# Kernel tuning notes

Hardware: AMD Instinct MI355X
Metric: run time of the kernel (lower is better)

Reference implementation:

```python
import math
import jax, jax.numpy as jnp
import numpy as np

D = 512; H = 8; N = 6; DFF = 2048; VS = 32000; VT = 32000
B = 4; S = 1024; T = 1024
EPS = 1e-5


def _pe(length, d):
    pos = jnp.arange(length, dtype=jnp.float32)[:, None]
    div = jnp.exp(jnp.arange(0, d, 2, dtype=jnp.float32) * (-math.log(10000.0) / d))
    pe = jnp.zeros((length, d), jnp.float32)
    pe = pe.at[:, 0::2].set(jnp.sin(pos * div)).at[:, 1::2].set(jnp.cos(pos * div))
    return pe  # [L, D]


def _ln(x, g, b):
    m = x.mean(-1, keepdims=True)
    v = ((x - m) ** 2).mean(-1, keepdims=True)
    return (x - m) / jnp.sqrt(v + EPS) * g + b


def _mha(xq, xkv, w, b, mask):
    # w: [4, D, D], b: [4, D]; mask broadcastable to [B, H, Sq, Sk]
    nb, sq, d = xq.shape
    dk = d // H
    def proj(x, i):
        return (x @ w[i] + b[i]).reshape(x.shape[0], x.shape[1], H, dk).transpose(0, 2, 1, 3)
    q, k, v = proj(xq, 0), proj(xkv, 1), proj(xkv, 2)
    scores = jnp.einsum('bhqd,bhkd->bhqk', q, k) / math.sqrt(dk)
    scores = jnp.where(mask == 0, -1e9, scores)
    p = jax.nn.softmax(scores, axis=-1)
    o = jnp.einsum('bhqk,bhkd->bhqd', p, v).transpose(0, 2, 1, 3).reshape(nb, sq, d)
    return o @ w[3] + b[3]


def _ffn(x, w1, b1, w2, b2):
    return jax.nn.relu(x @ w1 + b1) @ w2 + b2


def _forward(src_emb, tgt_emb,
             enc_attn_w, enc_attn_b, enc_ffn_w1, enc_ffn_b1, enc_ffn_w2, enc_ffn_b2,
             enc_ln_g, enc_ln_b, enc_fg, enc_fb,
             dec_self_w, dec_self_b, dec_src_w, dec_src_b,
             dec_ffn_w1, dec_ffn_b1, dec_ffn_w2, dec_ffn_b2,
             dec_ln_g, dec_ln_b, dec_fg, dec_fb,
             gen_w, gen_b,
             src, tgt, src_mask, tgt_mask):
    # embed + positional encoding (dropout off: eval mode)
    x = src_emb[src] + _pe(src.shape[1], D)[None]
    for i in range(N):
        a = _mha(x, x, enc_attn_w[i], enc_attn_b[i], src_mask)
        x = _ln(x + a, enc_ln_g[i, 0], enc_ln_b[i, 0])
        f = _ffn(x, enc_ffn_w1[i], enc_ffn_b1[i], enc_ffn_w2[i], enc_ffn_b2[i])
        x = _ln(x + f, enc_ln_g[i, 1], enc_ln_b[i, 1])
    memory = _ln(x, enc_fg, enc_fb)

    y = tgt_emb[tgt] + _pe(tgt.shape[1], D)[None]
    for i in range(N):
        a = _mha(y, y, dec_self_w[i], dec_self_b[i], tgt_mask)
        y = _ln(y + a, dec_ln_g[i, 0], dec_ln_b[i, 0])
        a = _mha(y, memory, dec_src_w[i], dec_src_b[i], src_mask)
        y = _ln(y + a, dec_ln_g[i, 1], dec_ln_b[i, 1])
        f = _ffn(y, dec_ffn_w1[i], dec_ffn_b1[i], dec_ffn_w2[i], dec_ffn_b2[i])
        y = _ln(y + f, dec_ln_g[i, 2], dec_ln_b[i, 2])
    y = _ln(y, dec_fg, dec_fb)
    return y @ gen_w + gen_b  # [B, T, VT]


def setup_inputs():
    key = jax.random.key(0)
    ks = iter(jax.random.split(key, 48))
    def w(*shape):
        return jax.random.normal(next(ks), shape, dtype=jnp.float32) * 0.02
    inp = {}
    inp['src_emb'] = w(VS, D)
    inp['tgt_emb'] = w(VT, D)
    inp['enc_attn_w'] = w(N, 4, D, D)
    inp['enc_attn_b'] = jnp.zeros((N, 4, D), jnp.float32)
    inp['enc_ffn_w1'] = w(N, D, DFF)
    inp['enc_ffn_b1'] = jnp.zeros((N, DFF), jnp.float32)
    inp['enc_ffn_w2'] = w(N, DFF, D)
    inp['enc_ffn_b2'] = jnp.zeros((N, D), jnp.float32)
    inp['enc_ln_g'] = jnp.ones((N, 2, D), jnp.float32)
    inp['enc_ln_b'] = jnp.zeros((N, 2, D), jnp.float32)
    inp['enc_fg'] = jnp.ones((D,), jnp.float32)
    inp['enc_fb'] = jnp.zeros((D,), jnp.float32)
    inp['dec_self_w'] = w(N, 4, D, D)
    inp['dec_self_b'] = jnp.zeros((N, 4, D), jnp.float32)
    inp['dec_src_w'] = w(N, 4, D, D)
    inp['dec_src_b'] = jnp.zeros((N, 4, D), jnp.float32)
    inp['dec_ffn_w1'] = w(N, D, DFF)
    inp['dec_ffn_b1'] = jnp.zeros((N, DFF), jnp.float32)
    inp['dec_ffn_w2'] = w(N, DFF, D)
    inp['dec_ffn_b2'] = jnp.zeros((N, D), jnp.float32)
    inp['dec_ln_g'] = jnp.ones((N, 3, D), jnp.float32)
    inp['dec_ln_b'] = jnp.zeros((N, 3, D), jnp.float32)
    inp['dec_fg'] = jnp.ones((D,), jnp.float32)
    inp['dec_fb'] = jnp.zeros((D,), jnp.float32)
    inp['gen_w'] = w(D, VT)
    inp['gen_b'] = jnp.zeros((VT,), jnp.float32)
    inp['src'] = jax.random.randint(next(ks), (B, S), 0, VS)
    inp['tgt'] = jax.random.randint(next(ks), (B, T), 0, VT)
    inp['src_mask'] = jnp.ones((B, 1, 1, S), jnp.int32)
    inp['tgt_mask'] = jnp.tril(jnp.ones((T, T), jnp.int32))[None, None]  # causal [1,1,T,T]
    return inp


def reference(src_emb, tgt_emb, enc_attn_w, enc_attn_b, enc_ffn_w1, enc_ffn_b1,
              enc_ffn_w2, enc_ffn_b2, enc_ln_g, enc_ln_b, enc_fg, enc_fb,
              dec_self_w, dec_self_b, dec_src_w, dec_src_b,
              dec_ffn_w1, dec_ffn_b1, dec_ffn_w2, dec_ffn_b2,
              dec_ln_g, dec_ln_b, dec_fg, dec_fb, gen_w, gen_b,
              src, tgt, src_mask, tgt_mask):
    return _forward(src_emb, tgt_emb, enc_attn_w, enc_attn_b, enc_ffn_w1, enc_ffn_b1,
                    enc_ffn_w2, enc_ffn_b2, enc_ln_g, enc_ln_b, enc_fg, enc_fb,
                    dec_self_w, dec_self_b, dec_src_w, dec_src_b,
                    dec_ffn_w1, dec_ffn_b1, dec_ffn_w2, dec_ffn_b2,
                    dec_ln_g, dec_ln_b, dec_fg, dec_fb, gen_w, gen_b,
                    src, tgt, src_mask, tgt_mask)
```

## Files before the change

kernel.cpp:

```cpp
#include <hip/hip_runtime.h>


typedef __bf16 bf16x8 __attribute__((ext_vector_type(8)));
typedef __bf16 bf16x4 __attribute__((ext_vector_type(4)));
typedef float  f32x4  __attribute__((ext_vector_type(4)));

__device__ __forceinline__ void gload_lds16(const void* g, void* l) {
  __builtin_amdgcn_global_load_lds((__attribute__((address_space(1))) void*)g,
                                   (__attribute__((address_space(3))) void*)l,
                                   16, 0, 0);
}

__device__ __forceinline__ void hard_barrier() {
  asm volatile("" ::: "memory");
  __builtin_amdgcn_sched_barrier(0);
  __builtin_amdgcn_s_barrier();
  __builtin_amdgcn_sched_barrier(0);
  asm volatile("" ::: "memory");
}

__global__ __launch_bounds__(512, 2)
void gemm256_kernel(const __bf16* __restrict__ A, int lda,
                    const __bf16* __restrict__ BT, int ldb,
                    float* __restrict__ C, int ldc,
                    const float* __restrict__ bias, int K)
{
  __shared__ char ldsraw[131072];
  const int tid  = threadIdx.x;
  const int lane = tid & 63, wid = tid >> 6;
  const int wr = wid >> 2, wc = wid & 3;
  const int bm = blockIdx.x * 256, bn = blockIdx.y * 256;

  auto stage = [&](int slot, int kt) {
    const char* Ag = (const char*)A;
    const char* Bg = (const char*)BT;
    char* base = ldsraw + slot * 65536;
    const long long k0b = (long long)kt * 128;
#pragma unroll
    for (int i = 0; i < 4; i++) {
      int t = tid + i * 512;
      int row = t >> 3, cb = (t & 7) << 4;
      int src = cb ^ ((row & 7) << 4);
      gload_lds16(Ag + ((long long)(bm + row) * lda) * 2 + k0b + src, base + t * 16);
    }
#pragma unroll
    for (int i = 0; i < 4; i++) {
      int t = tid + i * 512;
      int row = t >> 3, cb = (t & 7) << 4;
      int src = cb ^ ((row & 7) << 4);
      gload_lds16(Bg + ((long long)(bn + row) * ldb) * 2 + k0b + src,
                  base + 32768 + t * 16);
    }
  };

  f32x4 acc[8][4] = {};
  const int NT = K / 64;

  stage(0, 0);
  stage(1, 1);

  for (int kt = 0; kt < NT; kt++) {
    if (kt < NT - 1) {
      asm volatile("s_waitcnt vmcnt(8)" ::: "memory");
    } else {
      asm volatile("s_waitcnt vmcnt(0)" ::: "memory");
    }
    hard_barrier();
    const char* sA = ldsraw + (kt & 1) * 65536;
    const char* sB = sA + 32768;
#pragma unroll
    for (int q = 0; q < 4; q++) {
      const int qr = q >> 1, qc = q & 1;
      bf16x8 af[4][2], bf[2][2];
#pragma unroll
      for (int i = 0; i < 4; i++) {
        int row = wr * 128 + (qr * 4 + i) * 16 + (lane & 15);
#pragma unroll
        for (int kk = 0; kk < 2; kk++) {
          int g = kk * 64 + (lane >> 4) * 16;
          af[i][kk] = *(const bf16x8*)(sA + row * 128 + (g ^ ((row & 7) << 4)));
        }
      }
#pragma unroll
      for (int j = 0; j < 2; j++) {
        int row = wc * 64 + (qc * 2 + j) * 16 + (lane & 15);
#pragma unroll
        for (int kk = 0; kk < 2; kk++) {
          int g = kk * 64 + (lane >> 4) * 16;
          bf[j][kk] = *(const bf16x8*)(sB + row * 128 + (g ^ ((row & 7) << 4)));
        }
      }
      __builtin_amdgcn_s_barrier();
      asm volatile("s_waitcnt lgkmcnt(0)" ::: "memory");
      __builtin_amdgcn_sched_barrier(0);
      __builtin_amdgcn_s_setprio(1);
#pragma unroll
      for (int kk = 0; kk < 2; kk++)
#pragma unroll
        for (int i = 0; i < 4; i++)
#pragma unroll
          for (int j = 0; j < 2; j++)
            acc[qr * 4 + i][qc * 2 + j] = __builtin_amdgcn_mfma_f32_16x16x32_bf16(
                af[i][kk], bf[j][kk], acc[qr * 4 + i][qc * 2 + j], 0, 0, 0);
      __builtin_amdgcn_s_setprio(0);
    }
    hard_barrier();
    if (kt + 2 < NT) stage(kt & 1, kt + 2);
  }

  float* ct = (float*)ldsraw;
#pragma unroll
  for (int c = 0; c < 4; c++) {
    __syncthreads();
    if (wr == (c >> 1)) {
      const int ib = (c & 1) * 4;
#pragma unroll
      for (int i = 0; i < 4; i++) {
#pragma unroll
        for (int j = 0; j < 4; j++) {
          int lrow = i * 16 + (lane >> 4) * 4;
          int lcol = wc * 64 + j * 16 + (lane & 15);
          float bv = bias[bn + lcol];
#pragma unroll
          for (int r = 0; r < 4; r++)
            ct[(lrow + r) * 260 + lcol] = acc[ib + i][j][r] + bv;
        }
      }
    }
    __syncthreads();
#pragma unroll
    for (int it = 0; it < 8; it++) {
      int idx = tid + it * 512;
      int row = idx >> 6, c4 = (idx & 63) * 4;
      f32x4 v = *(const f32x4*)(ct + row * 260 + c4);
      *(f32x4*)(C + (long long)(bm + c * 64 + row) * ldc + bn + c4) = v;
    }
  }
}

template<int EPI>
__global__ __launch_bounds__(256)
void gemm2_kernel(const __bf16* __restrict__ A, const __bf16* __restrict__ Akv,
                  int lda,
                  const __bf16* __restrict__ BT, int ldb,
                  void* __restrict__ Cv, int ldc,
                  const float* __restrict__ bias, int K,
                  __bf16* __restrict__ qb, __bf16* __restrict__ kb,
                  __bf16* __restrict__ vt)
{
  constexpr int BM = 128, BN = 128, BK = 64;
  constexpr int WM = 64, WN = 64, FM = 4, FN = 4;
  constexpr int SLOT = 2 * BM * BK;
  __shared__ char ldsraw[65536];
  __bf16* lds = (__bf16*)ldsraw;
  const int tid  = threadIdx.x;
  const int lane = tid & 63, wave = tid >> 6;
  const int wr = wave >> 1, wc = wave & 1;
  const int bm = blockIdx.x * BM, bn = blockIdx.y * BN;
  const __bf16* Ause = (EPI == 2 && blockIdx.y >= 4) ? Akv : A;

  auto stage = [&](int slot, int kt) {
    const char* Ag = (const char*)Ause;
    const char* Bg = (const char*)BT;
    char* base = (char*)(lds + slot * SLOT);
    const long long k0b = (long long)kt * (BK * 2);
#pragma unroll
    for (int i = 0; i < 4; i++) {
      int t = tid + i * 256;
      int row = t >> 3, cb = (t & 7) << 4;
      int src = cb ^ ((row & 7) << 4);
      gload_lds16(Ag + ((long long)(bm + row) * lda) * 2 + k0b + src, base + t * 16);
    }
#pragma unroll
    for (int i = 0; i < 4; i++) {
      int t = tid + i * 256;
      int row = t >> 3, cb = (t & 7) << 4;
      int src = cb ^ ((row & 7) << 4);
      gload_lds16(Bg + ((long long)(bn + row) * ldb) * 2 + k0b + src,
                  base + BM * BK * 2 + t * 16);
    }
  };

  f32x4 acc[FM][FN] = {};
  const int NT = K / BK;

  stage(0, 0);
  stage(1, 1);

  for (int t = 0; t < NT; t++) {
    if (t < NT - 1) {
      asm volatile("s_waitcnt vmcnt(8)" ::: "memory");
    } else {
      asm volatile("s_waitcnt vmcnt(0)" ::: "memory");
    }
    hard_barrier();
    const char* sA = (const char*)(lds + (t & 1) * SLOT);
    const char* sB = sA + BM * BK * 2;
#pragma unroll
    for (int kk = 0; kk < 2; kk++) {
      const int g = kk * 64 + (lane >> 4) * 16;
      bf16x8 af[FM], bfr[FN];
#pragma unroll
      for (int i = 0; i < FM; i++) {
        int row = wr * WM + i * 16 + (lane & 15);
        af[i] = *(const bf16x8*)(sA + row * 128 + (g ^ ((row & 7) << 4)));
      }
#pragma unroll
      for (int j = 0; j < FN; j++) {
        int row = wc * WN + j * 16 + (lane & 15);
        bfr[j] = *(const bf16x8*)(sB + row * 128 + (g ^ ((row & 7) << 4)));
      }
      __builtin_amdgcn_s_setprio(1);
#pragma unroll
      for (int i = 0; i < FM; i++)
#pragma unroll
        for (int j = 0; j < FN; j++)
          acc[i][j] = __builtin_amdgcn_mfma_f32_16x16x32_bf16(af[i], bfr[j], acc[i][j], 0, 0, 0);
      __builtin_amdgcn_s_setprio(0);
    }
    hard_barrier();
    if (t + 2 < NT) stage(t & 1, t + 2);
  }

#pragma unroll
  for (int i = 0; i < FM; i++) {
#pragma unroll
    for (int j = 0; j < FN; j++) {
      int row0 = bm + wr * WM + i * 16 + (lane >> 4) * 4;
      int col  = bn + wc * WN + j * 16 + (lane & 15);
      float bv = bias ? bias[col] : 0.f;
      if constexpr (EPI == 2) {
        int z = col >> 9;
        int cw = col & 511;
        int b = row0 >> 10, s = row0 & 1023;
        int h = cw >> 6, dk = cw & 63;
        long long bh = b * 8 + h;
        if (z == 2) {
          bf16x4 vv;
#pragma unroll
          for (int r = 0; r < 4; r++) vv[r] = (__bf16)(acc[i][j][r] + bv);
          *(bf16x4*)(vt + (bh << 16) + (dk << 10) + s) = vv;
        } else {
          __bf16* dst = (z == 0) ? qb : kb;
          float sc = (z == 0) ? 0.125f : 1.0f;
#pragma unroll
          for (int r = 0; r < 4; r++)
            dst[(bh << 16) + ((long long)(s + r) << 6) + dk] = (__bf16)((acc[i][j][r] + bv) * sc);
        }
      } else if constexpr (EPI == 1) {
        __bf16* C = (__bf16*)Cv;
#pragma unroll
        for (int r = 0; r < 4; r++)
          C[(long long)(row0 + r) * ldc + col] = (__bf16)fmaxf(acc[i][j][r] + bv, 0.f);
      } else {
        float* C = (float*)Cv;
#pragma unroll
        for (int r = 0; r < 4; r++)
          C[(long long)(row0 + r) * ldc + col] = acc[i][j][r] + bv;
      }
    }
  }
}

__global__ __launch_bounds__(256)
void gemm_kernel(const __bf16* __restrict__ A, int lda,
                 const __bf16* __restrict__ BT, int ldb,
                 float* __restrict__ C, int ldc,
                 const float* __restrict__ bias, int K)
{
  constexpr int BM = 128, BN = 64, BK = 64;
  constexpr int WM = 64, WN = 32, FM = 4, FN = 2;
  constexpr int LA = (BM * BK) / 2048;
  constexpr int LB = (BN * BK) / 2048;
  constexpr int SLOT = (BM + BN) * BK;
  __shared__ __bf16 lds[3 * SLOT];
  const int tid  = threadIdx.x;
  const int lane = tid & 63, wave = tid >> 6;
  const int wr = wave >> 1, wc = wave & 1;
  const int bm = blockIdx.x * BM, bn = blockIdx.y * BN;

  auto stage = [&](int slot, int kt) {
    const char* Ag = (const char*)A;
    const char* Bg = (const char*)BT;
    char* base = (char*)(lds + slot * SLOT);
    const long long k0b = (long long)kt * (BK * 2);
#pragma unroll
    for (int i = 0; i < LA; i++) {
      int t = tid + i * 256;
      int row = t >> 3, cb = (t & 7) << 4;
      int src = cb ^ ((row & 7) << 4);
      gload_lds16(Ag + ((long long)(bm + row) * lda) * 2 + k0b + src, base + t * 16);
    }
#pragma unroll
    for (int i = 0; i < LB; i++) {
      int t = tid + i * 256;
      int row = t >> 3, cb = (t & 7) << 4;
      int src = cb ^ ((row & 7) << 4);
      gload_lds16(Bg + ((long long)(bn + row) * ldb) * 2 + k0b + src,
                  base + BM * BK * 2 + t * 16);
    }
  };

  f32x4 acc[FM][FN] = {};
  const int NT = K / BK;

  stage(0, 0);
  stage(1, 1);

  for (int t = 0; t < NT; t++) {
    if (t < NT - 1) {
      asm volatile("s_waitcnt vmcnt(6)" ::: "memory");
    } else {
      asm volatile("s_waitcnt vmcnt(0)" ::: "memory");
    }
    hard_barrier();
    if (t + 2 < NT) stage((t + 2) % 3, t + 2);
    const char* sA = (const char*)(lds + (t % 3) * SLOT);
    const char* sB = sA + BM * BK * 2;
#pragma unroll
    for (int kk = 0; kk < 2; kk++) {
      const int g = kk * 64 + (lane >> 4) * 16;
      bf16x8 af[FM], bfr[FN];
#pragma unroll
      for (int i = 0; i < FM; i++) {
        int row = wr * WM + i * 16 + (lane & 15);
        af[i] = *(const bf16x8*)(sA + row * 128 + (g ^ ((row & 7) << 4)));
      }
#pragma unroll
      for (int j = 0; j < FN; j++) {
        int row = wc * WN + j * 16 + (lane & 15);
        bfr[j] = *(const bf16x8*)(sB + row * 128 + (g ^ ((row & 7) << 4)));
      }
      __builtin_amdgcn_s_setprio(1);
#pragma unroll
      for (int i = 0; i < FM; i++)
#pragma unroll
        for (int j = 0; j < FN; j++)
          acc[i][j] = __builtin_amdgcn_mfma_f32_16x16x32_bf16(af[i], bfr[j], acc[i][j], 0, 0, 0);
      __builtin_amdgcn_s_setprio(0);
    }
  }

#pragma unroll
  for (int i = 0; i < FM; i++) {
#pragma unroll
    for (int j = 0; j < FN; j++) {
      int row0 = bm + wr * WM + i * 16 + (lane >> 4) * 4;
      int col  = bn + wc * WN + j * 16 + (lane & 15);
      float bv = bias ? bias[col] : 0.f;
#pragma unroll
      for (int r = 0; r < 4; r++)
        C[(long long)(row0 + r) * ldc + col] = acc[i][j][r] + bv;
    }
  }
}

template<int CAUSAL>
__global__ __launch_bounds__(256)
void flash_kernel(const __bf16* __restrict__ qb, const __bf16* __restrict__ kb,
                  const __bf16* __restrict__ vt, const int* __restrict__ smask,
                  __bf16* __restrict__ Ob)
{
  __shared__ __bf16 lK[2 * 128 * 64];
  __shared__ __bf16 lV[2 * 64 * 128];
  __shared__ __bf16 lP[4][16 * 128];
  const int bh = blockIdx.y;
  const int b = bh >> 3, h = bh & 7;
  const int q0 = blockIdx.x * 64;
  const int tid = threadIdx.x, lane = tid & 63, w = tid >> 6;
  const char* kh = (const char*)(kb + ((long long)bh << 16));
  const char* vh = (const char*)(vt + ((long long)bh << 16));

  auto stageKV = [&](int buf, int t) {
    int k0 = t * 128;
#pragma unroll
    for (int i = 0; i < 4; i++) {
      int c = tid + i * 256;
      int row = c >> 3, cb = (c & 7) << 4;
      int cl = cb ^ ((row & 7) << 4);
      gload_lds16(kh + (long long)(k0 + row) * 128 + cl, (char*)lK + buf * 16384 + c * 16);
    }
#pragma unroll
    for (int i = 0; i < 4; i++) {
      int c = tid + i * 256;
      int row = c >> 4, cb = (c & 15) << 4;
      int cl = cb ^ ((row & 7) << 4);
      gload_lds16(vh + (long long)row * 2048 + (long long)k0 * 2 + cl, (char*)lV + buf * 16384 + c * 16);
    }
  };

  bf16x8 qa[2];
  {
    const __bf16* qrow = qb + ((long long)bh << 16)
                       + (long long)(q0 + w * 16 + (lane & 15)) * 64 + (lane >> 4) * 8;
    qa[0] = *(const bf16x8*)(qrow);
    qa[1] = *(const bf16x8*)(qrow + 32);
  }
  f32x4 oacc[4] = {};
  float m[4], l[4];
#pragma unroll
  for (int r = 0; r < 4; r++) { m[r] = -3e38f; l[r] = 0.f; }

  const int nt = CAUSAL ? (blockIdx.x / 2 + 1) : 8;
  char* lPw = (char*)lP + w * 4096;

  stageKV(0, 0);
  if (nt > 1) stageKV(1, 1);

  for (int t = 0; t < nt; t++) {
    const int k0 = t * 128;
    if (t < nt - 1) {
      asm volatile("s_waitcnt vmcnt(8)" ::: "memory");
    } else {
      asm volatile("s_waitcnt vmcnt(0)" ::: "memory");
    }
    hard_barrier();
    char* cK = (char*)lK + (t & 1) * 16384;
    char* cV = (char*)lV + (t & 1) * 16384;

    f32x4 sf[8];
#pragma unroll
    for (int f = 0; f < 8; f++) {
      int row = f * 16 + (lane & 15);
      f32x4 s = {};
#pragma unroll
      for (int ks = 0; ks < 2; ks++) {
        int cb = ks * 64 + (lane >> 4) * 16;
        bf16x8 kf = *(const bf16x8*)(cK + row * 128 + (cb ^ ((row & 7) << 4)));
        s = __builtin_amdgcn_mfma_f32_16x16x32_bf16(qa[ks], kf, s, 0, 0, 0);
      }
      sf[f] = s;
    }

    if (!CAUSAL) {
#pragma unroll
      for (int f = 0; f < 8; f++) {
        if (smask[b * 1024 + k0 + f * 16 + (lane & 15)] == 0) {
#pragma unroll
          for (int r = 0; r < 4; r++) sf[f][r] = -1e30f;
        }
      }
    } else if (t == nt - 1) {
#pragma unroll
      for (int f = 0; f < 8; f++) {
        int kc = k0 + f * 16 + (lane & 15);
#pragma unroll
        for (int r = 0; r < 4; r++) {
          int qr = q0 + w * 16 + (lane >> 4) * 4 + r;
          if (kc > qr) sf[f][r] = -1e30f;
        }
      }
    }

    float mt[4];
#pragma unroll
    for (int r = 0; r < 4; r++) {
      float v = sf[0][r];
#pragma unroll
      for (int f = 1; f < 8; f++) v = fmaxf(v, sf[f][r]);
      mt[r] = v;
    }
#pragma unroll
    for (int o = 1; o < 16; o <<= 1)
#pragma unroll
      for (int r = 0; r < 4; r++) mt[r] = fmaxf(mt[r], __shfl_xor(mt[r], o));

    bool need = false;
#pragma unroll
    for (int r = 0; r < 4; r++) need = need || (mt[r] > m[r] + 8.f);
    if (__any(need)) {
      float mn[4], cr[4];
#pragma unroll
      for (int r = 0; r < 4; r++) {
        mn[r] = fmaxf(m[r], mt[r]);
        cr[r] = __expf(m[r] - mn[r]);
        m[r]  = mn[r];
        l[r] *= cr[r];
      }
#pragma unroll
      for (int d = 0; d < 4; d++)
#pragma unroll
        for (int r = 0; r < 4; r++) oacc[d][r] *= cr[r];
    }
    float rs[4] = {0.f, 0.f, 0.f, 0.f};
#pragma unroll
    for (int f = 0; f < 8; f++)
#pragma unroll
      for (int r = 0; r < 4; r++) {
        float p = __expf(sf[f][r] - m[r]);
        sf[f][r] = p;
        rs[r] += p;
      }
#pragma unroll
    for (int o = 1; o < 16; o <<= 1)
#pragma unroll
      for (int r = 0; r < 4; r++) rs[r] += __shfl_xor(rs[r], o);
#pragma unroll
    for (int r = 0; r < 4; r++) l[r] += rs[r];

#pragma unroll
    for (int f = 0; f < 8; f++) {
      int colB = f * 32 + (lane & 15) * 2;
#pragma unroll
      for (int r = 0; r < 4; r++) {
        int row = (lane >> 4) * 4 + r;
        *(__bf16*)(lPw + row * 256 + (colB ^ ((row & 7) << 4))) = (__bf16)sf[f][r];
      }
    }
    asm volatile("s_waitcnt lgkmcnt(0)" ::: "memory");

#pragma unroll
    for (int ks = 0; ks < 4; ks++) {
      int prow = lane & 15;
      int cb = ks * 64 + (lane >> 4) * 16;
      bf16x8 pa = *(const bf16x8*)(lPw + prow * 256 + (cb ^ ((prow & 7) << 4)));
#pragma unroll
      for (int d = 0; d < 4; d++) {
        int vrow = d * 16 + (lane & 15);
        bf16x8 vf = *(const bf16x8*)(cV + vrow * 256 + (cb ^ ((vrow & 7) << 4)));
        oacc[d] = __builtin_amdgcn_mfma_f32_16x16x32_bf16(pa, vf, oacc[d], 0, 0, 0);
      }
    }
    hard_barrier();
    if (t + 2 < nt) stageKV(t & 1, t + 2);
  }

  float inv[4];
#pragma unroll
  for (int r = 0; r < 4; r++) inv[r] = 1.f / l[r];
#pragma unroll
  for (int d = 0; d < 4; d++)
#pragma unroll
    for (int r = 0; r < 4; r++) {
      long long row = b * 1024 + q0 + w * 16 + (lane >> 4) * 4 + r;
      Ob[row * 512 + h * 64 + d * 16 + (lane & 15)] = (__bf16)(oacc[d][r] * inv[r]);
    }
}

__global__ void transpose_w_kernel(const float* __restrict__ W, __bf16* __restrict__ WT,
                                   int K, int N)
{
  __shared__ float t[32][33];
  long long mz = (long long)blockIdx.z * K * N;
  W += mz; WT += mz;
  int n0 = blockIdx.x * 32, k0 = blockIdx.y * 32;
  int tx = threadIdx.x, ty = threadIdx.y;
#pragma unroll
  for (int i = 0; i < 32; i += 8)
    t[ty + i][tx] = W[(long long)(k0 + ty + i) * N + (n0 + tx)];
  __syncthreads();
#pragma unroll
  for (int i = 0; i < 32; i += 8)
    WT[(long long)(n0 + ty + i) * K + (k0 + tx)] = (__bf16)t[tx][ty + i];
}

__global__ void embed_kernel(const float* __restrict__ emb, const int* __restrict__ idx,
                             __bf16* __restrict__ Xb)
{
  int row = blockIdx.x;
  int s   = row & 1023;
  int tok = idx[row];
  int d0  = threadIdx.x * 4;
  float4 e = *(const float4*)(emb + (long long)tok * 512 + d0);
  const float* ep = (const float*)&e;
  bf16x4 ob;
#pragma unroll
  for (int j = 0; j < 4; j++) {
    int d = d0 + j;
    float div = expf((float)(d & ~1) * (-9.210340371976184f / 512.f));
    float ang = (float)s * div;
    float pe  = (d & 1) ? cosf(ang) : sinf(ang);
    ob[j] = (__bf16)(ep[j] + pe);
  }
  *(bf16x4*)(Xb + (long long)row * 512 + d0) = ob;
}

__global__ void ln_kernel(const __bf16* __restrict__ Xin, const float* __restrict__ Rin,
                          const float* __restrict__ g, const float* __restrict__ b,
                          __bf16* __restrict__ Xbout)
{
  int row = blockIdx.x, lane = threadIdx.x;
  long long base = (long long)row * 512 + lane * 8;
  bf16x8 xv = *(const bf16x8*)(Xin + base);
  float x[8];
#pragma unroll
  for (int i = 0; i < 8; i++) x[i] = (float)xv[i];
  if (Rin) {
    float4 r0 = *(const float4*)(Rin + base);
    float4 r1 = *(const float4*)(Rin + base + 4);
    x[0] += r0.x; x[1] += r0.y; x[2] += r0.z; x[3] += r0.w;
    x[4] += r1.x; x[5] += r1.y; x[6] += r1.z; x[7] += r1.w;
  }
  float s = 0.f;
#pragma unroll
  for (int i = 0; i < 8; i++) s += x[i];
#pragma unroll
  for (int o = 32; o > 0; o >>= 1) s += __shfl_xor(s, o);
  float mean = s * (1.f / 512.f);
  float v = 0.f;
#pragma unroll
  for (int i = 0; i < 8; i++) { x[i] -= mean; v += x[i] * x[i]; }
#pragma unroll
  for (int o = 32; o > 0; o >>= 1) v += __shfl_xor(v, o);
  float inv = rsqrtf(v * (1.f / 512.f) + 1e-5f);
  int d0 = lane * 8;
  float gg[8], bb[8];
  *(float4*)gg       = *(const float4*)(g + d0);
  *(float4*)(gg + 4) = *(const float4*)(g + d0 + 4);
  *(float4*)bb       = *(const float4*)(b + d0);
  *(float4*)(bb + 4) = *(const float4*)(b + d0 + 4);
  bf16x8 yb;
#pragma unroll
  for (int i = 0; i < 8; i++)
    yb[i] = (__bf16)(x[i] * inv * gg[i] + bb[i]);
  *(bf16x8*)(Xbout + base) = yb;
}

extern "C" void kernel_launch(void* const* d_in, const int* in_sizes, int n_in,
                              void* d_out, int out_size, void* d_ws, size_t ws_size,
                              hipStream_t stream)
{
  (void)in_sizes; (void)n_in; (void)out_size; (void)ws_size;
  const float* src_emb    = (const float*)d_in[0];
  const float* tgt_emb    = (const float*)d_in[1];
  const float* enc_attn_w = (const float*)d_in[2];
  const float* enc_attn_b = (const float*)d_in[3];
  const float* enc_ffn_w1 = (const float*)d_in[4];
  const float* enc_ffn_b1 = (const float*)d_in[5];
  const float* enc_ffn_w2 = (const float*)d_in[6];
  const float* enc_ffn_b2 = (const float*)d_in[7];
  const float* enc_ln_g   = (const float*)d_in[8];
  const float* enc_ln_b   = (const float*)d_in[9];
  const float* enc_fg     = (const float*)d_in[10];
  const float* enc_fb     = (const float*)d_in[11];
  const float* dec_self_w = (const float*)d_in[12];
  const float* dec_self_b = (const float*)d_in[13];
  const float* dec_src_w  = (const float*)d_in[14];
  const float* dec_src_b  = (const float*)d_in[15];
  const float* dec_ffn_w1 = (const float*)d_in[16];
  const float* dec_ffn_b1 = (const float*)d_in[17];
  const float* dec_ffn_w2 = (const float*)d_in[18];
  const float* dec_ffn_b2 = (const float*)d_in[19];
  const float* dec_ln_g   = (const float*)d_in[20];
  const float* dec_ln_b   = (const float*)d_in[21];
  const float* dec_fg     = (const float*)d_in[22];
  const float* dec_fb     = (const float*)d_in[23];
  const float* gen_w      = (const float*)d_in[24];
  const float* gen_b      = (const float*)d_in[25];
  const int*   src        = (const int*)d_in[26];
  const int*   tgt        = (const int*)d_in[27];
  const int*   src_mask   = (const int*)d_in[28];

  float* out = (float*)d_out;

  char* wp = (char*)d_ws;
  auto alloc = [&](size_t bytes) { void* p = (void*)wp; wp += (bytes + 255) & ~(size_t)255; return p; };
  __bf16* TWea = (__bf16*)alloc(24ull * 262144 * 2);
  __bf16* TWe1 = (__bf16*)alloc(6ull * 1048576 * 2);
  __bf16* TWe2 = (__bf16*)alloc(6ull * 1048576 * 2);
  __bf16* TWds = (__bf16*)alloc(24ull * 262144 * 2);
  __bf16* TWdx = (__bf16*)alloc(24ull * 262144 * 2);
  __bf16* TWd1 = (__bf16*)alloc(6ull * 1048576 * 2);
  __bf16* TWd2 = (__bf16*)alloc(6ull * 1048576 * 2);
  __bf16* Xb   = (__bf16*)alloc(4096ull * 512 * 2);
  __bf16* MEMb = (__bf16*)alloc(4096ull * 512 * 2);
  float*  R    = (float*) alloc(4096ull * 512 * 4);
  __bf16* qb   = (__bf16*)alloc(32ull * 1024 * 64 * 2);
  __bf16* kb   = (__bf16*)alloc(32ull * 1024 * 64 * 2);
  __bf16* vt   = (__bf16*)alloc(32ull * 1024 * 64 * 2);
  __bf16* Ob   = (__bf16*)alloc(4096ull * 512 * 2);
  __bf16* Fb   = qb;
  __bf16* GENT = TWea;

  transpose_w_kernel<<<dim3(16, 16, 24), dim3(32, 8), 0, stream>>>(enc_attn_w, TWea, 512, 512);
  transpose_w_kernel<<<dim3(64, 16, 6),  dim3(32, 8), 0, stream>>>(enc_ffn_w1, TWe1, 512, 2048);
  transpose_w_kernel<<<dim3(16, 64, 6),  dim3(32, 8), 0, stream>>>(enc_ffn_w2, TWe2, 2048, 512);
  transpose_w_kernel<<<dim3(16, 16, 24), dim3(32, 8), 0, stream>>>(dec_self_w, TWds, 512, 512);
  transpose_w_kernel<<<dim3(16, 16, 24), dim3(32, 8), 0, stream>>>(dec_src_w,  TWdx, 512, 512);
  transpose_w_kernel<<<dim3(64, 16, 6),  dim3(32, 8), 0, stream>>>(dec_ffn_w1, TWd1, 512, 2048);
  transpose_w_kernel<<<dim3(16, 64, 6),  dim3(32, 8), 0, stream>>>(dec_ffn_w2, TWd2, 2048, 512);

  auto attention = [&](const __bf16* wt, const float* bptr, int causal,
                       const __bf16* Aq, const __bf16* Akv) {
    gemm2_kernel<2><<<dim3(32, 12), 256, 0, stream>>>(
        Aq, Akv, 512, wt, 512, nullptr, 0, bptr, 512, qb, kb, vt);
    if (causal)
      flash_kernel<1><<<dim3(16, 32), 256, 0, stream>>>(qb, kb, vt, nullptr, Ob);
    else
      flash_kernel<0><<<dim3(16, 32), 256, 0, stream>>>(qb, kb, vt, src_mask, Ob);
    gemm_kernel<<<dim3(32, 8), 256, 0, stream>>>(
        Ob, 512, wt + 3 * 262144, 512, R, 512, bptr + 3 * 512, 512);
  };

  auto ffn = [&](const __bf16* w1t, const float* b1, const __bf16* w2t, const float* b2) {
    gemm2_kernel<1><<<dim3(32, 16), 256, 0, stream>>>(
        Xb, Xb, 512, w1t, 512, Fb, 2048, b1, 512, nullptr, nullptr, nullptr);
    gemm_kernel<<<dim3(32, 8), 256, 0, stream>>>(
        Fb, 2048, w2t, 2048, R, 512, b2, 2048);
  };

  embed_kernel<<<4096, 128, 0, stream>>>(src_emb, src, Xb);
  for (int i = 0; i < 6; i++) {
    attention(TWea + (long long)i * 1048576, enc_attn_b + i * 2048, 0, Xb, Xb);
    ln_kernel<<<4096, 64, 0, stream>>>(Xb, R, enc_ln_g + i * 1024, enc_ln_b + i * 1024, Xb);
    ffn(TWe1 + (long long)i * 1048576, enc_ffn_b1 + i * 2048,
        TWe2 + (long long)i * 1048576, enc_ffn_b2 + i * 512);
    ln_kernel<<<4096, 64, 0, stream>>>(Xb, R, enc_ln_g + i * 1024 + 512, enc_ln_b + i * 1024 + 512, Xb);
  }
  ln_kernel<<<4096, 64, 0, stream>>>(Xb, nullptr, enc_fg, enc_fb, MEMb);

  transpose_w_kernel<<<dim3(1000, 16, 1), dim3(32, 8), 0, stream>>>(gen_w, GENT, 512, 32000);

  embed_kernel<<<4096, 128, 0, stream>>>(tgt_emb, tgt, Xb);
  for (int i = 0; i < 6; i++) {
    attention(TWds + (long long)i * 1048576, dec_self_b + i * 2048, 1, Xb, Xb);
    ln_kernel<<<4096, 64, 0, stream>>>(Xb, R, dec_ln_g + i * 1536, dec_ln_b + i * 1536, Xb);

    attention(TWdx + (long long)i * 1048576, dec_src_b + i * 2048, 0, Xb, MEMb);
    ln_kernel<<<4096, 64, 0, stream>>>(Xb, R, dec_ln_g + i * 1536 + 512, dec_ln_b + i * 1536 + 512, Xb);

    ffn(TWd1 + (long long)i * 1048576, dec_ffn_b1 + i * 2048,
        TWd2 + (long long)i * 1048576, dec_ffn_b2 + i * 512);
    ln_kernel<<<4096, 64, 0, stream>>>(Xb, R, dec_ln_g + i * 1536 + 1024, dec_ln_b + i * 1536 + 1024, Xb);
  }
  ln_kernel<<<4096, 64, 0, stream>>>(Xb, nullptr, dec_fg, dec_fb, Xb);

  gemm256_kernel<<<dim3(16, 125), 512, 0, stream>>>(
      Xb, 512, GENT, 512, out, 32000, gen_b, 512);
}
```

Measured before the change: 1.836 ms.

## Fuse residual add into output GEMM epilogue with bf16 sum buffer

The attention output projection and FFN second GEMM now add the residual (Xb) in their epilogue and write a bf16 sum buffer, instead of writing a float32 partial result that layernorm later re-adds. LayerNorm drops its residual input and processes four rows per 256-thread block. The causal flash kernel reverses query-tile order for half the heads so work per tile mixes across the grid. These changes cut memory traffic and improve load balance, but the residual sum is rounded to bf16 before layernorm, which slightly lowers precision.

```diff
diff --git a/kernel.cpp b/kernel.cpp
--- a/kernel.cpp
+++ b/kernel.cpp
@@ -247,16 +247,11 @@
           for (int r = 0; r < 4; r++)
             dst[(bh << 16) + ((long long)(s + r) << 6) + dk] = (__bf16)((acc[i][j][r] + bv) * sc);
         }
-      } else if constexpr (EPI == 1) {
+      } else {
         __bf16* C = (__bf16*)Cv;
 #pragma unroll
         for (int r = 0; r < 4; r++)
           C[(long long)(row0 + r) * ldc + col] = (__bf16)fmaxf(acc[i][j][r] + bv, 0.f);
-      } else {
-        float* C = (float*)Cv;
-#pragma unroll
-        for (int r = 0; r < 4; r++)
-          C[(long long)(row0 + r) * ldc + col] = acc[i][j][r] + bv;
       }
     }
   }
@@ -265,7 +260,8 @@
 __global__ __launch_bounds__(256)
 void gemm_kernel(const __bf16* __restrict__ A, int lda,
                  const __bf16* __restrict__ BT, int ldb,
-                 float* __restrict__ C, int ldc,
+                 const __bf16* __restrict__ Xbase,
+                 __bf16* __restrict__ Xs, int ldc,
                  const float* __restrict__ bias, int K)
 {
   constexpr int BM = 128, BN = 64, BK = 64;
@@ -347,10 +343,12 @@
     for (int j = 0; j < FN; j++) {
       int row0 = bm + wr * WM + i * 16 + (lane >> 4) * 4;
       int col  = bn + wc * WN + j * 16 + (lane & 15);
-      float bv = bias ? bias[col] : 0.f;
-#pragma unroll
-      for (int r = 0; r < 4; r++)
-        C[(long long)(row0 + r) * ldc + col] = acc[i][j][r] + bv;
+      float bv = bias[col];
+#pragma unroll
+      for (int r = 0; r < 4; r++) {
+        long long off = (long long)(row0 + r) * ldc + col;
+        Xs[off] = (__bf16)(acc[i][j][r] + bv + (float)Xbase[off]);
+      }
     }
   }
 }
@@ -366,7 +364,9 @@
   __shared__ __bf16 lP[4][16 * 128];
   const int bh = blockIdx.y;
   const int b = bh >> 3, h = bh & 7;
-  const int q0 = blockIdx.x * 64;
+  const int qt = CAUSAL ? ((blockIdx.y < 16) ? blockIdx.x : 15 - blockIdx.x)
+                        : blockIdx.x;
+  const int q0 = qt * 64;
   const int tid = threadIdx.x, lane = tid & 63, w = tid >> 6;
   const char* kh = (const char*)(kb + ((long long)bh << 16));
   const char* vh = (const char*)(vt + ((long long)bh << 16));
@@ -401,7 +401,7 @@
 #pragma unroll
   for (int r = 0; r < 4; r++) { m[r] = -3e38f; l[r] = 0.f; }
 
-  const int nt = CAUSAL ? (blockIdx.x / 2 + 1) : 8;
+  const int nt = CAUSAL ? (qt / 2 + 1) : 8;
   char* lPw = (char*)lP + w * 4096;
 
   stageKV(0, 0);
@@ -575,22 +575,18 @@
   *(bf16x4*)(Xb + (long long)row * 512 + d0) = ob;
 }
 
-__global__ void ln_kernel(const __bf16* __restrict__ Xin, const float* __restrict__ Rin,
-                          const float* __restrict__ g, const float* __restrict__ b,
-                          __bf16* __restrict__ Xbout)
+__global__ __launch_bounds__(256)
+void ln_kernel(const __bf16* __restrict__ Xin,
+               const float* __restrict__ g, const float* __restrict__ b,
+               __bf16* __restrict__ Xbout)
 {
-  int row = blockIdx.x, lane = threadIdx.x;
+  int row = blockIdx.x * 4 + (threadIdx.x >> 6);
+  int lane = threadIdx.x & 63;
   long long base = (long long)row * 512 + lane * 8;
   bf16x8 xv = *(const bf16x8*)(Xin + base);
   float x[8];
 #pragma unroll
   for (int i = 0; i < 8; i++) x[i] = (float)xv[i];
-  if (Rin) {
-    float4 r0 = *(const float4*)(Rin + base);
-    float4 r1 = *(const float4*)(Rin + base + 4);
-    x[0] += r0.x; x[1] += r0.y; x[2] += r0.z; x[3] += r0.w;
-    x[4] += r1.x; x[5] += r1.y; x[6] += r1.z; x[7] += r1.w;
-  }
   float s = 0.f;
 #pragma unroll
   for (int i = 0; i < 8; i++) s += x[i];
@@ -664,7 +660,7 @@
   __bf16* TWd2 = (__bf16*)alloc(6ull * 1048576 * 2);
   __bf16* Xb   = (__bf16*)alloc(4096ull * 512 * 2);
   __bf16* MEMb = (__bf16*)alloc(4096ull * 512 * 2);
-  float*  R    = (float*) alloc(4096ull * 512 * 4);
+  __bf16* Xs   = (__bf16*)alloc(4096ull * 512 * 2);
   __bf16* qb   = (__bf16*)alloc(32ull * 1024 * 64 * 2);
   __bf16* kb   = (__bf16*)alloc(32ull * 1024 * 64 * 2);
   __bf16* vt   = (__bf16*)alloc(32ull * 1024 * 64 * 2);
@@ -689,41 +685,41 @@
     else
       flash_kernel<0><<<dim3(16, 32), 256, 0, stream>>>(qb, kb, vt, src_mask, Ob);
     gemm_kernel<<<dim3(32, 8), 256, 0, stream>>>(
-        Ob, 512, wt + 3 * 262144, 512, R, 512, bptr + 3 * 512, 512);
+        Ob, 512, wt + 3 * 262144, 512, Xb, Xs, 512, bptr + 3 * 512, 512);
   };
 
   auto ffn = [&](const __bf16* w1t, const float* b1, const __bf16* w2t, const float* b2) {
     gemm2_kernel<1><<<dim3(32, 16), 256, 0, stream>>>(
         Xb, Xb, 512, w1t, 512, Fb, 2048, b1, 512, nullptr, nullptr, nullptr);
     gemm_kernel<<<dim3(32, 8), 256, 0, stream>>>(
-        Fb, 2048, w2t, 2048, R, 512, b2, 2048);
+        Fb, 2048, w2t, 2048, Xb, Xs, 512, b2, 2048);
   };
 
   embed_kernel<<<4096, 128, 0, stream>>>(src_emb, src, Xb);
   for (int i = 0; i < 6; i++) {
     attention(TWea + (long long)i * 1048576, enc_attn_b + i * 2048, 0, Xb, Xb);
-    ln_kernel<<<4096, 64, 0, stream>>>(Xb, R, enc_ln_g + i * 1024, enc_ln_b + i * 1024, Xb);
+    ln_kernel<<<1024, 256, 0, stream>>>(Xs, enc_ln_g + i * 1024, enc_ln_b + i * 1024, Xb);
     ffn(TWe1 + (long long)i * 1048576, enc_ffn_b1 + i * 2048,
         TWe2 + (long long)i * 1048576, enc_ffn_b2 + i * 512);
-    ln_kernel<<<4096, 64, 0, stream>>>(Xb, R, enc_ln_g + i * 1024 + 512, enc_ln_b + i * 1024 + 512, Xb);
-  }
-  ln_kernel<<<4096, 64, 0, stream>>>(Xb, nullptr, enc_fg, enc_fb, MEMb);
+    ln_kernel<<<1024, 256, 0, stream>>>(Xs, enc_ln_g + i * 1024 + 512, enc_ln_b + i * 1024 + 512, Xb);
+  }
+  ln_kernel<<<1024, 256, 0, stream>>>(Xb, enc_fg, enc_fb, MEMb);
 
   transpose_w_kernel<<<dim3(1000, 16, 1), dim3(32, 8), 0, stream>>>(gen_w, GENT, 512, 32000);
 
   embed_kernel<<<4096, 128, 0, stream>>>(tgt_emb, tgt, Xb);
   for (int i = 0; i < 6; i++) {
     attention(TWds + (long long)i * 1048576, dec_self_b + i * 2048, 1, Xb, Xb);
-    ln_kernel<<<4096, 64, 0, stream>>>(Xb, R, dec_ln_g + i * 1536, dec_ln_b + i * 1536, Xb);
+    ln_kernel<<<1024, 256, 0, stream>>>(Xs, dec_ln_g + i * 1536, dec_ln_b + i * 1536, Xb);
 
     attention(TWdx + (long long)i * 1048576, dec_src_b + i * 2048, 0, Xb, MEMb);
-    ln_kernel<<<4096, 64, 0, stream>>>(Xb, R, dec_ln_g + i * 1536 + 512, dec_ln_b + i * 1536 + 512, Xb);
+    ln_kernel<<<1024, 256, 0, stream>>>(Xs, dec_ln_g + i * 1536 + 512, dec_ln_b + i * 1536 + 512, Xb);
 
     ffn(TWd1 + (long long)i * 1048576, dec_ffn_b1 + i * 2048,
         TWd2 + (long long)i * 1048576, dec_ffn_b2 + i * 512);
-    ln_kernel<<<4096, 64, 0, stream>>>(Xb, R, dec_ln_g + i * 1536 + 1024, dec_ln_b + i * 1536 + 1024, Xb);
-  }
-  ln_kernel<<<4096, 64, 0, stream>>>(Xb, nullptr, dec_fg, dec_fb, Xb);
+    ln_kernel<<<1024, 256, 0, stream>>>(Xs, dec_ln_g + i * 1536 + 1024, dec_ln_b + i * 1536 + 1024, Xb);
+  }
+  ln_kernel<<<1024, 256, 0, stream>>>(Xb, dec_fg, dec_fb, Xb);
 
   gemm256_kernel<<<dim3(16, 125), 512, 0, stream>>>(
       Xb, 512, GENT, 512, out, 32000, gen_b, 512);
```

New measurement: 1.783 ms. 2.9% less time.
